# Kernel optimization log

Hardware: AMD Instinct MI355X
Metric: run time of the kernel (lower is better)

## Reference

```python
import jax, jax.numpy as jnp
import numpy as np


def setup_inputs() -> dict:
    key = jax.random.key(0)
    k1, k2 = jax.random.split(key)
    x = jax.random.normal(k1, (8, 256, 16, 32, 32), dtype=jnp.float32)
    mem = jax.random.normal(k2, (200, 256), dtype=jnp.float32)
    return {"x": x, "mem": mem}


def reference(x, mem):
    B, C, T, H, W = x.shape
    # (B, N, C) tokens where N = T*H*W
    x_flat = x.reshape(B, C, -1).transpose(0, 2, 1)
    # scores against memory slots: (B, N, mem_dim)
    att = jax.nn.softmax(jnp.einsum('bnc,mc->bnm', x_flat, mem), axis=-1)
    # read from memory: (B, N, C)
    mem_out = jnp.einsum('bnm,mc->bnc', att, mem)
    return mem_out.transpose(0, 2, 1).reshape(B, C, T, H, W)
```

## Files before the change

### kernel.cpp

```cpp
#include <hip/hip_runtime.h>

typedef _Float16 h16x8 __attribute__((ext_vector_type(8)));
typedef float f32x4 __attribute__((ext_vector_type(4)));

#define MFMA16F(a, b, c) __builtin_amdgcn_mfma_f32_16x16x32_f16((a), (b), (c), 0, 0, 0)

#define GLOAD16(gp, lp)                                                        \
  __builtin_amdgcn_global_load_lds(                                            \
      (const __attribute__((address_space(1))) unsigned int*)(gp),             \
      (__attribute__((address_space(3))) unsigned int*)(lp), 16, 0, 0)

#define FENCE() __builtin_amdgcn_sched_barrier(0)


__global__ __launch_bounds__(256) void prep_mem(const float* __restrict__ mem,
                                                unsigned short* __restrict__ M16,
                                                unsigned short* __restrict__ MT16) {
  const int s = blockIdx.x;
  const int c = threadIdx.x;
  const float v = (s < 200) ? mem[s * 256 + c] : 0.0f;
  const _Float16 hv = (_Float16)v;
  const unsigned short hb = __builtin_bit_cast(unsigned short, hv);
  M16[s * 256 + c] = hb;
  const int ks = s >> 5, w = s & 31;
  const int t = w >> 4, hh = (w >> 2) & 3, rr = w & 3;
  MT16[c * 256 + (ks * 32 + hh * 8 + t * 4 + rr)] = hb;
}

__global__ __launch_bounds__(1024, 4) void fused_mem_attn(
    const float* __restrict__ x, const unsigned short* __restrict__ M16,
    const unsigned short* __restrict__ MT16, float* __restrict__ out) {
  __shared__ alignas(128) char lds[131072];

  const int tid = threadIdx.x;
  const int wave = tid >> 6;
  const int lane = tid & 63;
  const int t16 = lane & 15;
  const int h = lane >> 4;

  const int Lb = tid ^ ((tid >> 3) & 7);
  const int srcOff = (Lb >> 2) * 512 + (Lb & 3) * 16;
  const int q16 = ((((t16 << 2) + h) ^ (t16 >> 1)) << 4);

  const long gtok0 = (long)blockIdx.x * 256;
  const int b = (int)(gtok0 >> 14);
  const int bn0 = (int)(gtok0 & 16383);
  const float* xb = x + ((long)b << 22) + bn0 + (wave * 16 + t16);
  float* outB = out + ((long)b << 22) + bn0 + (wave * 16 + t16);

  const char* M16B = (const char*)M16;
  const char* MTB = (const char*)MT16;

#define XLOAD(ks)                                                              \
  _Pragma("unroll") for (int j = 0; j < 8; ++j) {                              \
    xr[(ks) % 3][j] = xb[(long)((ks) * 32 + h * 8 + j) << 14];                 \
  }

  float xr[3][8];
  f32x4 acc[14] = {};

#define COMPUTE(ks)                                                            \
  {                                                                            \
    if ((ks) < 6) XLOAD((ks) + 2);                                             \
    h16x8 xh, xl;                                                              \
    _Pragma("unroll") for (int j = 0; j < 8; ++j) {                            \
      const float f = xr[(ks) % 3][j];                                         \
      const _Float16 hi_ = (_Float16)f;                                        \
      xh[j] = hi_;                                                             \
      xl[j] = (_Float16)(f - (float)hi_);                                      \
    }                                                                          \
    const char* sb = lds + (ks) * 16384;                                       \
    __builtin_amdgcn_s_setprio(1);                                             \
    _Pragma("unroll") for (int tt = 0; tt < 13; ++tt) {                        \
      const h16x8 ah = *(const h16x8*)(sb + tt * 1024 + q16);                  \
      acc[tt] = MFMA16F(ah, xh, acc[tt]);                                      \
      acc[tt] = MFMA16F(ah, xl, acc[tt]);                                      \
    }                                                                          \
    __builtin_amdgcn_s_setprio(0);                                             \
    FENCE();                                                                   \
  }

  XLOAD(0);
  XLOAD(1);
#pragma unroll
  for (int ks = 0; ks < 8; ++ks)
    GLOAD16(M16B + srcOff + ks * 64, lds + ks * 16384 + tid * 16);
  __syncthreads();

  COMPUTE(0) COMPUTE(1) COMPUTE(2) COMPUTE(3)
  COMPUTE(4) COMPUTE(5) COMPUTE(6) COMPUTE(7)

  __syncthreads();

#pragma unroll
  for (int k = 0; k < 7; ++k)
    GLOAD16(MTB + srcOff + k * 64, lds + k * 16384 + tid * 16);

  float m = -3.0e38f;
#pragma unroll
  for (int tt = 0; tt < 12; ++tt)
#pragma unroll
    for (int r = 0; r < 4; ++r) m = fmaxf(m, acc[tt][r]);
#pragma unroll
  for (int r = 0; r < 4; ++r)
    if (192 + h * 4 + r < 200) m = fmaxf(m, acc[12][r]);
  m = fmaxf(m, __shfl_xor(m, 16, 64));
  m = fmaxf(m, __shfl_xor(m, 32, 64));
  float s = 0.f;
#pragma unroll
  for (int tt = 0; tt < 12; ++tt)
#pragma unroll
    for (int r = 0; r < 4; ++r) {
      const float p = __expf(acc[tt][r] - m);
      acc[tt][r] = p;
      s += p;
    }
#pragma unroll
  for (int r = 0; r < 4; ++r) {
    const bool ok = (192 + h * 4 + r) < 200;
    const float p = ok ? __expf(acc[12][r] - m) : 0.f;
    acc[12][r] = p;
    s += p;
  }
  s += __shfl_xor(s, 16, 64);
  s += __shfl_xor(s, 32, 64);
  const float inv = 1.f / s;

  h16x8 pb[7];
#pragma unroll
  for (int k = 0; k < 7; ++k)
#pragma unroll
    for (int j = 0; j < 4; ++j) {
      pb[k][j] = (_Float16)acc[2 * k][j];
      pb[k][j + 4] = (_Float16)acc[2 * k + 1][j];
    }

  __syncthreads();

#pragma unroll
  for (int ct = 0; ct < 16; ++ct) {
    f32x4 a2 = {0.f, 0.f, 0.f, 0.f};
    __builtin_amdgcn_s_setprio(1);
#pragma unroll
    for (int k = 0; k < 7; ++k) {
      const h16x8 at = *(const h16x8*)(lds + k * 16384 + ct * 1024 + q16);
      a2 = MFMA16F(at, pb[k], a2);
    }
    __builtin_amdgcn_s_setprio(0);
#pragma unroll
    for (int r = 0; r < 4; ++r)
      outB[(long)(ct * 16 + h * 4 + r) << 14] = a2[r] * inv;
  }
#undef XLOAD
#undef COMPUTE
}

extern "C" void kernel_launch(void* const* d_in, const int* in_sizes, int n_in,
                              void* d_out, int out_size, void* d_ws, size_t ws_size,
                              hipStream_t stream) {
  const float* x = (const float*)d_in[0];
  const float* mem = (const float*)d_in[1];
  float* out = (float*)d_out;

  unsigned short* M16 = (unsigned short*)d_ws;
  unsigned short* MT16 = M16 + 256 * 256;

  prep_mem<<<dim3(256), dim3(256), 0, stream>>>(mem, M16, MT16);
  fused_mem_attn<<<dim3(512), dim3(1024), 0, stream>>>(x, M16, MT16, out);
}
```

Baseline: 70.32 us.

## Swap MFMA operand roles in second GEMM for vectorized 16-byte output stores

The second GEMM now feeds the probabilities as the A operand and a pre-swizzled memory block as B. The accumulator layout then gives each lane four consecutive tokens, so each lane writes one f32x4 store instead of four scalar strided stores. Softmax normalization is folded into the fp16 conversion of the probabilities, and prep_mem writes a new LDS-ready layout so the loads and reads are linear. The cost is rounding inv*p to fp16 before the multiply, which slightly changes numerics.

```diff
diff --git a/kernel.cpp b/kernel.cpp
--- a/kernel.cpp
+++ b/kernel.cpp
@@ -15,21 +15,26 @@
 
 __global__ __launch_bounds__(256) void prep_mem(const float* __restrict__ mem,
                                                 unsigned short* __restrict__ M16,
-                                                unsigned short* __restrict__ MT16) {
+                                                unsigned short* __restrict__ MB) {
   const int s = blockIdx.x;
   const int c = threadIdx.x;
   const float v = (s < 200) ? mem[s * 256 + c] : 0.0f;
   const _Float16 hv = (_Float16)v;
   const unsigned short hb = __builtin_bit_cast(unsigned short, hv);
   M16[s * 256 + c] = hb;
-  const int ks = s >> 5, w = s & 31;
-  const int t = w >> 4, hh = (w >> 2) & 3, rr = w & 3;
-  MT16[c * 256 + (ks * 32 + hh * 8 + t * 4 + rr)] = hb;
+  if (s < 224) {
+    const int kk = s >> 5;
+    const int th = (s >> 4) & 1;
+    const int hh = (s >> 2) & 3;
+    const int rr = s & 3;
+    const int j = th * 4 + rr;
+    MB[kk * 8192 + (c >> 4) * 512 + hh * 128 + (c & 15) * 8 + j] = hb;
+  }
 }
 
 __global__ __launch_bounds__(1024, 4) void fused_mem_attn(
     const float* __restrict__ x, const unsigned short* __restrict__ M16,
-    const unsigned short* __restrict__ MT16, float* __restrict__ out) {
+    const unsigned short* __restrict__ MB, float* __restrict__ out) {
   __shared__ alignas(128) char lds[131072];
 
   const int tid = threadIdx.x;
@@ -46,10 +51,10 @@
   const int b = (int)(gtok0 >> 14);
   const int bn0 = (int)(gtok0 & 16383);
   const float* xb = x + ((long)b << 22) + bn0 + (wave * 16 + t16);
-  float* outB = out + ((long)b << 22) + bn0 + (wave * 16 + t16);
+  float* outT = out + ((long)b << 22) + bn0 + (wave * 16 + 4 * h) + ((long)t16 << 14);
 
   const char* M16B = (const char*)M16;
-  const char* MTB = (const char*)MT16;
+  const char* MBB = (const char*)MB;
 
 #define XLOAD(ks)                                                              \
   _Pragma("unroll") for (int j = 0; j < 8; ++j) {                              \
@@ -94,7 +99,7 @@
 
 #pragma unroll
   for (int k = 0; k < 7; ++k)
-    GLOAD16(MTB + srcOff + k * 64, lds + k * 16384 + tid * 16);
+    GLOAD16(MBB + k * 16384 + tid * 16, lds + k * 16384 + tid * 16);
 
   float m = -3.0e38f;
 #pragma unroll
@@ -126,14 +131,12 @@
   s += __shfl_xor(s, 32, 64);
   const float inv = 1.f / s;
 
-  h16x8 pb[7];
+  h16x8 pa[7];
 #pragma unroll
-  for (int k = 0; k < 7; ++k)
+  for (int kk = 0; kk < 7; ++kk)
 #pragma unroll
-    for (int j = 0; j < 4; ++j) {
-      pb[k][j] = (_Float16)acc[2 * k][j];
-      pb[k][j + 4] = (_Float16)acc[2 * k + 1][j];
-    }
+    for (int j = 0; j < 8; ++j)
+      pa[kk][j] = (_Float16)(inv * acc[2 * kk + (j >> 2)][j & 3]);
 
   __syncthreads();
 
@@ -142,14 +145,12 @@
     f32x4 a2 = {0.f, 0.f, 0.f, 0.f};
     __builtin_amdgcn_s_setprio(1);
 #pragma unroll
-    for (int k = 0; k < 7; ++k) {
-      const h16x8 at = *(const h16x8*)(lds + k * 16384 + ct * 1024 + q16);
-      a2 = MFMA16F(at, pb[k], a2);
+    for (int kk = 0; kk < 7; ++kk) {
+      const h16x8 bt = *(const h16x8*)(lds + kk * 16384 + ct * 1024 + lane * 16);
+      a2 = MFMA16F(pa[kk], bt, a2);
     }
     __builtin_amdgcn_s_setprio(0);
-#pragma unroll
-    for (int r = 0; r < 4; ++r)
-      outB[(long)(ct * 16 + h * 4 + r) << 14] = a2[r] * inv;
+    *(f32x4*)(outT + ((long)ct << 18)) = a2;
   }
 #undef XLOAD
 #undef COMPUTE
@@ -163,8 +164,8 @@
   float* out = (float*)d_out;
 
   unsigned short* M16 = (unsigned short*)d_ws;
-  unsigned short* MT16 = M16 + 256 * 256;
+  unsigned short* MB = M16 + 256 * 256;
 
-  prep_mem<<<dim3(256), dim3(256), 0, stream>>>(mem, M16, MT16);
-  fused_mem_attn<<<dim3(512), dim3(1024), 0, stream>>>(x, M16, MT16, out);
+  prep_mem<<<dim3(256), dim3(256), 0, stream>>>(mem, M16, MB);
+  fused_mem_attn<<<dim3(512), dim3(1024), 0, stream>>>(x, M16, MB, out);
 }
```

Result: faster. 68.50 us, median of 2 (-2.6%).
